# Kernel optimization log

Hardware: AMD Instinct MI355X
Metric: run time of the kernel (lower is better)

## Reference

```python
import jax, jax.numpy as jnp
import numpy as np

E, T, D, DFF = 8, 16384, 512, 2048  # experts, tokens, d_model, d_ff
ROUTE_P = 0.25  # ~ top_k=2 of E=8


def setup_inputs() -> dict:
    key = jax.random.key(0)
    k_x, k_m, k_w1, k_w2 = jax.random.split(key, 4)
    x = jax.random.normal(k_x, (T, D), dtype=jnp.float32)
    mask = jax.random.bernoulli(k_m, ROUTE_P, (E, T))  # bool [E, T]
    W1 = jax.random.normal(k_w1, (E, D, DFF), dtype=jnp.float32) * (1.0 / np.sqrt(D).astype(np.float32))
    b1 = jnp.zeros((E, DFF), dtype=jnp.float32)
    W2 = jax.random.normal(k_w2, (E, DFF, D), dtype=jnp.float32) * (1.0 / np.sqrt(DFF).astype(np.float32))
    b2 = jnp.zeros((E, D), dtype=jnp.float32)
    return {"x": x, "W1": W1, "b1": b1, "W2": W2, "b2": b2, "mask": mask}


def reference(x, W1, b1, W2, b2, mask):
    # vmapped per-expert FFN on shared tokens; mask zeroes non-routed tokens.
    # h: [E, T, DFF]
    h = jax.nn.gelu(jnp.einsum('td,edf->etf', x, W1) + b1[:, None, :])
    # y: [E, T, D]
    y = jnp.einsum('etf,efd->etd', h, W2) + b2[:, None, :]
    return jnp.where(mask[:, :, None], y, jnp.zeros((), dtype=y.dtype))
```

## Files before the change

kernel.cpp:

```cpp
#include <hip/hip_runtime.h>
#include <hip/hip_bf16.h>

#define NE 8
#define TOK 16384
#define ND 512
#define NF 2048
#define HP 4608
#define MT 36

typedef __attribute__((ext_vector_type(8))) short bf16x8;
typedef __attribute__((ext_vector_type(4))) float f32x4;
typedef unsigned short u16;
typedef unsigned long long u64;

__device__ __forceinline__ u16 f2bf(float f) {
  union { float f; unsigned u; } c; c.f = f;
  unsigned u = c.u;
  return (u16)((u + 0x7FFFu + ((u >> 16) & 1u)) >> 16);
}

__device__ __forceinline__ float gelu_fast(float x) {
  float x2 = x * x;
  float zp = x * __builtin_fmaf(0.10294325f, x2, 2.3022084f);
  float u = __builtin_amdgcn_exp2f(zp);
  float r = __builtin_amdgcn_rcpf(u + 1.0f);
  return x * (1.0f - r);
}

__device__ __forceinline__ void gl_lds16(const void* g, void* l) {
  __builtin_amdgcn_global_load_lds(
      (const __attribute__((address_space(1))) unsigned int*)g,
      (__attribute__((address_space(3))) unsigned int*)l, 16, 0, 0);
}

__device__ __forceinline__ int swzr(int row) { return ((row >> 1) & 3) << 4; }

__global__ void transpose_bf16(const float* __restrict__ in, u16* __restrict__ out,
                               int R, int C) {
  __shared__ float tile[32][33];
  int e = blockIdx.z;
  const float* ip = in + (size_t)e * R * C;
  u16* op = out + (size_t)e * R * C;
  int c0 = blockIdx.x * 32, r0 = blockIdx.y * 32;
  int tx = threadIdx.x & 31, ty = threadIdx.x >> 5;
  for (int i = 0; i < 32; i += 8)
    tile[ty + i][tx] = ip[(size_t)(r0 + ty + i) * C + (c0 + tx)];
  __syncthreads();
  for (int i = 0; i < 32; i += 8)
    op[(size_t)(c0 + ty + i) * R + (r0 + tx)] = f2bf(tile[tx][ty + i]);
}

__global__ void x_to_bf16(const float* __restrict__ x, u16* __restrict__ xbf) {
  int i = blockIdx.x * 256 + threadIdx.x;
  float4 v = ((const float4*)x)[i];
  union { u16 s[4]; u64 ll; } o;
  o.s[0] = f2bf(v.x); o.s[1] = f2bf(v.y); o.s[2] = f2bf(v.z); o.s[3] = f2bf(v.w);
  ((u64*)xbf)[i] = o.ll;
}

__global__ void zero_unmasked(const int* __restrict__ mask, float4* __restrict__ out4) {
  int row = blockIdx.x * 2 + (threadIdx.x >> 7);
  if (mask[row]) return;
  out4[(size_t)row * 128 + (threadIdx.x & 127)] = float4{0.f, 0.f, 0.f, 0.f};
}

__global__ void compact_mask(const int* __restrict__ mask, int* __restrict__ idx,
                             int* __restrict__ counts) {
  int e = blockIdx.x;
  __shared__ int wsum[4];
  __shared__ int base;
  if (threadIdx.x == 0) base = 0;
  const int* m = mask + (size_t)e * TOK;
  int lane = threadIdx.x & 63, w = threadIdx.x >> 6;
  for (int c0 = 0; c0 < TOK; c0 += 256) {
    __syncthreads();
    int i = c0 + threadIdx.x;
    int mi = (m[i] != 0);
    unsigned long long b = __ballot(mi);
    if (lane == 0) wsum[w] = __popcll(b);
    __syncthreads();
    int off = base;
    for (int ww = 0; ww < w; ww++) off += wsum[ww];
    off += __popcll(b & ((1ull << lane) - 1ull));
    if (mi) idx[(size_t)e * TOK + off] = i;
    __syncthreads();
    if (threadIdx.x == 0) base += wsum[0] + wsum[1] + wsum[2] + wsum[3];
  }
  __syncthreads();
  if (threadIdx.x == 0) counts[e] = base;
}

__launch_bounds__(256, 4)
__global__ void gemm1(const u16* __restrict__ xbf, const u16* __restrict__ W1t,
                      const float* __restrict__ b1f, const int* __restrict__ idx,
                      const int* __restrict__ counts, u16* __restrict__ h, int ebase) {
  const int BPE = MT * (NF / 128);
  int bid = blockIdx.x;
  int el = bid / BPE, r = bid % BPE;
  int n0 = (r / MT) * 128, m0 = (r % MT) * 128;
  int e = ebase + el;
  int cnt = counts[e];
  if (m0 >= cnt) return;

  __shared__ __align__(16) u16 As[2][4096];
  __shared__ __align__(16) u16 Bs[2][4096];

  int tid = threadIdx.x, lane = tid & 63, w = tid >> 6;
  int wm = w & 1, wn = w >> 1;
  int l15 = lane & 15, l4 = lane >> 4;
  const int* idxe = idx + (size_t)e * TOK;

  int srow = lane >> 2, scolb = (lane & 3) << 4;
  int ar0 = w * 16 + srow, ar1 = 64 + w * 16 + srow;
  int cm1 = cnt - 1;
  int t0 = idxe[m0 + ar0 <= cm1 ? m0 + ar0 : cm1];
  int t1 = idxe[m0 + ar1 <= cm1 ? m0 + ar1 : cm1];
  const char* xb = (const char*)xbf;
  const char* w1 = (const char*)W1t;
  size_t asrc0 = (size_t)t0 * 1024 + (scolb ^ swzr(ar0));
  size_t asrc1 = (size_t)t1 * 1024 + (scolb ^ swzr(ar1));
  size_t bsrc0 = ((size_t)e * NF + n0 + ar0) * 1024 + (scolb ^ swzr(ar0));
  size_t bsrc1 = ((size_t)e * NF + n0 + ar1) * 1024 + (scolb ^ swzr(ar1));

  int aoff[4], boff[4];
  #pragma unroll
  for (int i = 0; i < 4; i++) {
    int rowa = wm * 64 + i * 16 + l15;
    aoff[i] = rowa * 64 + ((l4 * 16) ^ swzr(rowa));
    int rowb = wn * 64 + i * 16 + l15;
    boff[i] = rowb * 64 + ((l4 * 16) ^ swzr(rowb));
  }

  auto STAGE = [&](int kb, int c) {
    char* ad = (char*)As + c * 8192 + w * 1024 + lane * 16;
    char* bd = (char*)Bs + c * 8192 + w * 1024 + lane * 16;
    gl_lds16(xb + asrc0 + kb * 64, ad);
    gl_lds16(xb + asrc1 + kb * 64, ad + 4096);
    gl_lds16(w1 + bsrc0 + kb * 64, bd);
    gl_lds16(w1 + bsrc1 + kb * 64, bd + 4096);
  };

  f32x4 acc[4][4];
  #pragma unroll
  for (int i = 0; i < 4; i++)
    #pragma unroll
    for (int j = 0; j < 4; j++) acc[i][j] = (f32x4)(0.0f);

  STAGE(0, 0);
  __syncthreads();
  #pragma unroll
  for (int kb = 0; kb < 16; ++kb) {
    int cur = kb & 1;
    if (kb < 15) STAGE(kb + 1, cur ^ 1);
    const char* ab = (const char*)As + cur * 8192;
    const char* bb = (const char*)Bs + cur * 8192;
    bf16x8 a[4], b[4];
    #pragma unroll
    for (int i = 0; i < 4; i++) a[i] = *(const bf16x8*)(ab + aoff[i]);
    #pragma unroll
    for (int j = 0; j < 4; j++) b[j] = *(const bf16x8*)(bb + boff[j]);
    #pragma unroll
    for (int i = 0; i < 4; i++)
      #pragma unroll
      for (int j = 0; j < 4; j++)
        acc[i][j] = __builtin_amdgcn_mfma_f32_16x16x32_bf16(a[i], b[j], acc[i][j], 0, 0, 0);
    __syncthreads();
  }

  float b1v[4];
  #pragma unroll
  for (int j = 0; j < 4; j++) b1v[j] = b1f[(size_t)e * NF + n0 + wn * 64 + j * 16 + l15];
  #pragma unroll
  for (int i = 0; i < 4; i++) {
    int trow = m0 + wm * 64 + i * 16 + l4 * 4;
    #pragma unroll
    for (int jj = 0; jj < 4; jj++) {
      u16* hrow = h + ((size_t)el * HP + trow + jj) * NF + n0;
      #pragma unroll
      for (int j = 0; j < 4; j++)
        hrow[wn * 64 + j * 16 + l15] = f2bf(gelu_fast(acc[i][j][jj] + b1v[j]));
    }
  }
}

__launch_bounds__(256, 4)
__global__ void gemm2(const u16* __restrict__ h, const u16* __restrict__ W2t,
                      const float* __restrict__ b2f, const int* __restrict__ idx,
                      const int* __restrict__ counts, float* __restrict__ out, int ebase) {
  const int BPE = MT * (ND / 128);
  int bid = blockIdx.x;
  int el = bid / BPE, r = bid % BPE;
  int n0 = (r / MT) * 128, m0 = (r % MT) * 128;
  int e = ebase + el;
  int cnt = counts[e];
  if (m0 >= cnt) return;

  __shared__ __align__(16) u16 As[2][4096];
  __shared__ __align__(16) u16 Bs[2][4096];

  int tid = threadIdx.x, lane = tid & 63, w = tid >> 6;
  int wm = w & 1, wn = w >> 1;
  int l15 = lane & 15, l4 = lane >> 4;
  const int* idxe = idx + (size_t)e * TOK;

  int srow = lane >> 2, scolb = (lane & 3) << 4;
  int ar0 = w * 16 + srow, ar1 = 64 + w * 16 + srow;
  const char* hb = (const char*)h;
  const char* w2 = (const char*)W2t;
  size_t asrc0 = ((size_t)el * HP + m0 + ar0) * 4096 + (scolb ^ swzr(ar0));
  size_t asrc1 = ((size_t)el * HP + m0 + ar1) * 4096 + (scolb ^ swzr(ar1));
  size_t bsrc0 = ((size_t)e * ND + n0 + ar0) * 4096 + (scolb ^ swzr(ar0));
  size_t bsrc1 = ((size_t)e * ND + n0 + ar1) * 4096 + (scolb ^ swzr(ar1));

  int aoff[4], boff[4];
  #pragma unroll
  for (int i = 0; i < 4; i++) {
    int rowa = wm * 64 + i * 16 + l15;
    aoff[i] = rowa * 64 + ((l4 * 16) ^ swzr(rowa));
    int rowb = wn * 64 + i * 16 + l15;
    boff[i] = rowb * 64 + ((l4 * 16) ^ swzr(rowb));
  }

  auto STAGE = [&](int kb, int c) {
    char* ad = (char*)As + c * 8192 + w * 1024 + lane * 16;
    char* bd = (char*)Bs + c * 8192 + w * 1024 + lane * 16;
    gl_lds16(hb + asrc0 + kb * 64, ad);
    gl_lds16(hb + asrc1 + kb * 64, ad + 4096);
    gl_lds16(w2 + bsrc0 + kb * 64, bd);
    gl_lds16(w2 + bsrc1 + kb * 64, bd + 4096);
  };

  f32x4 acc[4][4];
  #pragma unroll
  for (int i = 0; i < 4; i++)
    #pragma unroll
    for (int j = 0; j < 4; j++) acc[i][j] = (f32x4)(0.0f);

  STAGE(0, 0);
  __syncthreads();
  #pragma unroll 2
  for (int kb = 0; kb < 64; ++kb) {
    int cur = kb & 1;
    if (kb < 63) STAGE(kb + 1, cur ^ 1);
    const char* ab = (const char*)As + cur * 8192;
    const char* bb = (const char*)Bs + cur * 8192;
    bf16x8 a[4], b[4];
    #pragma unroll
    for (int i = 0; i < 4; i++) a[i] = *(const bf16x8*)(ab + aoff[i]);
    #pragma unroll
    for (int j = 0; j < 4; j++) b[j] = *(const bf16x8*)(bb + boff[j]);
    #pragma unroll
    for (int i = 0; i < 4; i++)
      #pragma unroll
      for (int j = 0; j < 4; j++)
        acc[i][j] = __builtin_amdgcn_mfma_f32_16x16x32_bf16(a[i], b[j], acc[i][j], 0, 0, 0);
    __syncthreads();
  }

  float b2v[4];
  #pragma unroll
  for (int j = 0; j < 4; j++) b2v[j] = b2f[(size_t)e * ND + n0 + wn * 64 + j * 16 + l15];
  #pragma unroll
  for (int i = 0; i < 4; i++) {
    #pragma unroll
    for (int jj = 0; jj < 4; jj++) {
      int row = m0 + wm * 64 + i * 16 + l4 * 4 + jj;
      if (row < cnt) {
        int tok = idxe[row];
        float* orow = out + ((size_t)e * TOK + tok) * ND + n0;
        #pragma unroll
        for (int j = 0; j < 4; j++)
          orow[wn * 64 + j * 16 + l15] = acc[i][j][jj] + b2v[j];
      }
    }
  }
}

extern "C" void kernel_launch(void* const* d_in, const int* in_sizes, int n_in,
                              void* d_out, int out_size, void* d_ws, size_t ws_size,
                              hipStream_t stream) {
  const float* x  = (const float*)d_in[0];
  const float* W1 = (const float*)d_in[1];
  const float* b1 = (const float*)d_in[2];
  const float* W2 = (const float*)d_in[3];
  const float* b2 = (const float*)d_in[4];
  const int* mask = (const int*)d_in[5];

  char* ws = (char*)d_ws;
  int* counts = (int*)ws;
  int* idx    = (int*)(ws + 1024);
  u16* W1t    = (u16*)(ws + 1024 + (size_t)NE * TOK * 4);
  u16* W2t    = W1t + (size_t)NE * NF * ND;
  u16* xbf    = W2t + (size_t)NE * ND * NF;
  u16* h      = xbf + (size_t)TOK * ND;

  zero_unmasked<<<dim3(NE * TOK / 2), dim3(256), 0, stream>>>(mask, (float4*)d_out);
  transpose_bf16<<<dim3(NF / 32, ND / 32, NE), dim3(256), 0, stream>>>(W1, W1t, ND, NF);
  transpose_bf16<<<dim3(ND / 32, NF / 32, NE), dim3(256), 0, stream>>>(W2, W2t, NF, ND);
  x_to_bf16<<<dim3(TOK * ND / 4 / 256), dim3(256), 0, stream>>>(x, xbf);
  compact_mask<<<dim3(NE), dim3(256), 0, stream>>>(mask, idx, counts);

  for (int p = 0; p < 2; p++) {
    gemm1<<<dim3(4 * MT * (NF / 128)), dim3(256), 0, stream>>>(
        xbf, W1t, b1, idx, counts, h, p * 4);
    gemm2<<<dim3(4 * MT * (ND / 128)), dim3(256), 0, stream>>>(
        h, W2t, b2, idx, counts, (float*)d_out, p * 4);
  }
}
```

Before: 373.1 us.

## Swap GEMM operand roles for vectorized epilogue stores and launch all experts at once

```diff
diff --git a/kernel.cpp b/kernel.cpp
--- a/kernel.cpp
+++ b/kernel.cpp
@@ -93,14 +93,13 @@
 __launch_bounds__(256, 4)
 __global__ void gemm1(const u16* __restrict__ xbf, const u16* __restrict__ W1t,
                       const float* __restrict__ b1f, const int* __restrict__ idx,
-                      const int* __restrict__ counts, u16* __restrict__ h, int ebase) {
-  const int BPE = MT * (NF / 128);
+                      const int* __restrict__ counts, u16* __restrict__ h) {
+  const int BPE = (NF / 128) * MT;
   int bid = blockIdx.x;
-  int el = bid / BPE, r = bid % BPE;
-  int n0 = (r / MT) * 128, m0 = (r % MT) * 128;
-  int e = ebase + el;
+  int e = bid / BPE, r = bid % BPE;
+  int f0 = (r / MT) * 128, t0 = (r % MT) * 128;
   int cnt = counts[e];
-  if (m0 >= cnt) return;
+  if (t0 >= cnt) return;
 
   __shared__ __align__(16) u16 As[2][4096];
   __shared__ __align__(16) u16 Bs[2][4096];
@@ -113,14 +112,14 @@
   int srow = lane >> 2, scolb = (lane & 3) << 4;
   int ar0 = w * 16 + srow, ar1 = 64 + w * 16 + srow;
   int cm1 = cnt - 1;
-  int t0 = idxe[m0 + ar0 <= cm1 ? m0 + ar0 : cm1];
-  int t1 = idxe[m0 + ar1 <= cm1 ? m0 + ar1 : cm1];
+  int tk0 = idxe[t0 + ar0 <= cm1 ? t0 + ar0 : cm1];
+  int tk1 = idxe[t0 + ar1 <= cm1 ? t0 + ar1 : cm1];
   const char* xb = (const char*)xbf;
   const char* w1 = (const char*)W1t;
-  size_t asrc0 = (size_t)t0 * 1024 + (scolb ^ swzr(ar0));
-  size_t asrc1 = (size_t)t1 * 1024 + (scolb ^ swzr(ar1));
-  size_t bsrc0 = ((size_t)e * NF + n0 + ar0) * 1024 + (scolb ^ swzr(ar0));
-  size_t bsrc1 = ((size_t)e * NF + n0 + ar1) * 1024 + (scolb ^ swzr(ar1));
+  size_t asrc0 = ((size_t)e * NF + f0 + ar0) * 1024 + (scolb ^ swzr(ar0));
+  size_t asrc1 = ((size_t)e * NF + f0 + ar1) * 1024 + (scolb ^ swzr(ar1));
+  size_t bsrc0 = (size_t)tk0 * 1024 + (scolb ^ swzr(ar0));
+  size_t bsrc1 = (size_t)tk1 * 1024 + (scolb ^ swzr(ar1));
 
   int aoff[4], boff[4];
   #pragma unroll
@@ -134,10 +133,10 @@
   auto STAGE = [&](int kb, int c) {
     char* ad = (char*)As + c * 8192 + w * 1024 + lane * 16;
     char* bd = (char*)Bs + c * 8192 + w * 1024 + lane * 16;
-    gl_lds16(xb + asrc0 + kb * 64, ad);
-    gl_lds16(xb + asrc1 + kb * 64, ad + 4096);
-    gl_lds16(w1 + bsrc0 + kb * 64, bd);
-    gl_lds16(w1 + bsrc1 + kb * 64, bd + 4096);
+    gl_lds16(w1 + asrc0 + kb * 64, ad);
+    gl_lds16(w1 + asrc1 + kb * 64, ad + 4096);
+    gl_lds16(xb + bsrc0 + kb * 64, bd);
+    gl_lds16(xb + bsrc1 + kb * 64, bd + 4096);
   };
 
   f32x4 acc[4][4];
@@ -167,18 +166,18 @@
     __syncthreads();
   }
 
-  float b1v[4];
-  #pragma unroll
-  for (int j = 0; j < 4; j++) b1v[j] = b1f[(size_t)e * NF + n0 + wn * 64 + j * 16 + l15];
   #pragma unroll
   for (int i = 0; i < 4; i++) {
-    int trow = m0 + wm * 64 + i * 16 + l4 * 4;
-    #pragma unroll
-    for (int jj = 0; jj < 4; jj++) {
-      u16* hrow = h + ((size_t)el * HP + trow + jj) * NF + n0;
+    int fb = f0 + wm * 64 + i * 16 + l4 * 4;
+    f32x4 bv = *(const f32x4*)(b1f + (size_t)e * NF + fb);
+    #pragma unroll
+    for (int j = 0; j < 4; j++) {
+      int t = t0 + wn * 64 + j * 16 + l15;
+      union { u16 s[4]; u64 ll; } pk;
       #pragma unroll
-      for (int j = 0; j < 4; j++)
-        hrow[wn * 64 + j * 16 + l15] = f2bf(gelu_fast(acc[i][j][jj] + b1v[j]));
+      for (int jj = 0; jj < 4; jj++)
+        pk.s[jj] = f2bf(gelu_fast(acc[i][j][jj] + bv[jj]));
+      *(u64*)(h + ((size_t)e * HP + t) * NF + fb) = pk.ll;
     }
   }
 }
@@ -186,14 +185,13 @@
 __launch_bounds__(256, 4)
 __global__ void gemm2(const u16* __restrict__ h, const u16* __restrict__ W2t,
                       const float* __restrict__ b2f, const int* __restrict__ idx,
-                      const int* __restrict__ counts, float* __restrict__ out, int ebase) {
-  const int BPE = MT * (ND / 128);
+                      const int* __restrict__ counts, float* __restrict__ out) {
+  const int BPE = (ND / 128) * MT;
   int bid = blockIdx.x;
-  int el = bid / BPE, r = bid % BPE;
-  int n0 = (r / MT) * 128, m0 = (r % MT) * 128;
-  int e = ebase + el;
+  int e = bid / BPE, r = bid % BPE;
+  int d0 = (r / MT) * 128, t0 = (r % MT) * 128;
   int cnt = counts[e];
-  if (m0 >= cnt) return;
+  if (t0 >= cnt) return;
 
   __shared__ __align__(16) u16 As[2][4096];
   __shared__ __align__(16) u16 Bs[2][4096];
@@ -207,10 +205,10 @@
   int ar0 = w * 16 + srow, ar1 = 64 + w * 16 + srow;
   const char* hb = (const char*)h;
   const char* w2 = (const char*)W2t;
-  size_t asrc0 = ((size_t)el * HP + m0 + ar0) * 4096 + (scolb ^ swzr(ar0));
-  size_t asrc1 = ((size_t)el * HP + m0 + ar1) * 4096 + (scolb ^ swzr(ar1));
-  size_t bsrc0 = ((size_t)e * ND + n0 + ar0) * 4096 + (scolb ^ swzr(ar0));
-  size_t bsrc1 = ((size_t)e * ND + n0 + ar1) * 4096 + (scolb ^ swzr(ar1));
+  size_t asrc0 = ((size_t)e * ND + d0 + ar0) * 4096 + (scolb ^ swzr(ar0));
+  size_t asrc1 = ((size_t)e * ND + d0 + ar1) * 4096 + (scolb ^ swzr(ar1));
+  size_t bsrc0 = ((size_t)e * HP + t0 + ar0) * 4096 + (scolb ^ swzr(ar0));
+  size_t bsrc1 = ((size_t)e * HP + t0 + ar1) * 4096 + (scolb ^ swzr(ar1));
 
   int aoff[4], boff[4];
   #pragma unroll
@@ -224,10 +222,10 @@
   auto STAGE = [&](int kb, int c) {
     char* ad = (char*)As + c * 8192 + w * 1024 + lane * 16;
     char* bd = (char*)Bs + c * 8192 + w * 1024 + lane * 16;
-    gl_lds16(hb + asrc0 + kb * 64, ad);
-    gl_lds16(hb + asrc1 + kb * 64, ad + 4096);
-    gl_lds16(w2 + bsrc0 + kb * 64, bd);
-    gl_lds16(w2 + bsrc1 + kb * 64, bd + 4096);
+    gl_lds16(w2 + asrc0 + kb * 64, ad);
+    gl_lds16(w2 + asrc1 + kb * 64, ad + 4096);
+    gl_lds16(hb + bsrc0 + kb * 64, bd);
+    gl_lds16(hb + bsrc1 + kb * 64, bd + 4096);
   };
 
   f32x4 acc[4][4];
@@ -257,20 +255,19 @@
     __syncthreads();
   }
 
-  float b2v[4];
-  #pragma unroll
-  for (int j = 0; j < 4; j++) b2v[j] = b2f[(size_t)e * ND + n0 + wn * 64 + j * 16 + l15];
   #pragma unroll
   for (int i = 0; i < 4; i++) {
-    #pragma unroll
-    for (int jj = 0; jj < 4; jj++) {
-      int row = m0 + wm * 64 + i * 16 + l4 * 4 + jj;
-      if (row < cnt) {
-        int tok = idxe[row];
-        float* orow = out + ((size_t)e * TOK + tok) * ND + n0;
+    int db = d0 + wm * 64 + i * 16 + l4 * 4;
+    f32x4 b2v = *(const f32x4*)(b2f + (size_t)e * ND + db);
+    #pragma unroll
+    for (int j = 0; j < 4; j++) {
+      int t = t0 + wn * 64 + j * 16 + l15;
+      if (t < cnt) {
+        int tok = idxe[t];
+        f32x4 v;
         #pragma unroll
-        for (int j = 0; j < 4; j++)
-          orow[wn * 64 + j * 16 + l15] = acc[i][j][jj] + b2v[j];
+        for (int jj = 0; jj < 4; jj++) v[jj] = acc[i][j][jj] + b2v[jj];
+        *(f32x4*)(out + ((size_t)e * TOK + tok) * ND + db) = v;
       }
     }
   }
@@ -300,10 +297,7 @@
   x_to_bf16<<<dim3(TOK * ND / 4 / 256), dim3(256), 0, stream>>>(x, xbf);
   compact_mask<<<dim3(NE), dim3(256), 0, stream>>>(mask, idx, counts);
 
-  for (int p = 0; p < 2; p++) {
-    gemm1<<<dim3(4 * MT * (NF / 128)), dim3(256), 0, stream>>>(
-        xbf, W1t, b1, idx, counts, h, p * 4);
-    gemm2<<<dim3(4 * MT * (ND / 128)), dim3(256), 0, stream>>>(
-        h, W2t, b2, idx, counts, (float*)d_out, p * 4);
-  }
-}
+  gemm1<<<dim3(NE * (NF / 128) * MT), dim3(256), 0, stream>>>(xbf, W1t, b1, idx, counts, h);
+  gemm2<<<dim3(NE * (ND / 128) * MT), dim3(256), 0, stream>>>(h, W2t, b2, idx, counts,
+                                                              (float*)d_out);
+}
```

Result: slower. 382.4 us (+2.5%).
